# Optimization experiments

Hardware: AMD Instinct MI355X
Metric: run time of the kernel (lower is better)

Reference implementation:

```python
import jax, jax.numpy as jnp
import numpy as np

N, K, C, J = 200000, 512, 64, 32  # nodes, node feature dim, mixture components (Ccurr+1), macrostates


def setup_inputs() -> dict:
    key = jax.random.key(0)
    k0, k1, k2, k3, k4, k5 = jax.random.split(key, 6)
    x = jax.random.normal(k0, (N, K), dtype=jnp.float32)
    macrostate = jax.random.randint(k1, (N,), 0, J)  # macrostate_assignments (int, constant)
    # Gaussian emission parameters theta[k] (diagonal covariance), one per component
    mu = jax.random.normal(k2, (C, K), dtype=jnp.float32)
    log_var = 0.1 * jax.random.normal(k3, (C, K), dtype=jnp.float32)
    # stick-breaking weights beta (positive, sums to 1) and CRF counts njk (non-negative)
    b = jax.random.uniform(k4, (C,), dtype=jnp.float32) + 1e-3
    beta = b / b.sum()
    njk = 100.0 * jax.random.uniform(k5, (J, C), dtype=jnp.float32)
    alpha = jnp.float32(1.0)
    return {"x": x, "mu": mu, "log_var": log_var, "beta": beta, "njk": njk,
            "alpha": alpha, "macrostate": macrostate}


def reference(x, mu, log_var, beta, njk, alpha, macrostate):
    # f_X_theta_log[u, k] = theta[k].get_data_log_likelihood(x[u])  (diagonal Gaussian)
    # expand ||(x - mu)/sigma||^2 as a GEMM to stay compute-bound:
    inv_var = jnp.exp(-log_var)                                   # [C, K]
    quad = ((x * x) @ inv_var.T                                   # [N, C]
            - 2.0 * (x @ (mu * inv_var).T)
            + jnp.sum(mu * mu * inv_var, axis=1))
    log_norm = jnp.sum(log_var, axis=1) + x.shape[1] * jnp.log(2.0 * jnp.pi)
    f_log = -0.5 * (quad + log_norm)                              # [N, C]
    # per-node: unnorm_log_p_zu = log(alpha*beta + njk[j]) + f_X_theta_log[u]
    prior_log = jnp.log(alpha * beta[None, :] + njk)              # [J, C]
    logits = prior_log[macrostate] + f_log                        # [N, C]
    # p_zu via numerically-stable softmax; posterior_matrix[u] += p_zu
    posterior = jax.nn.softmax(logits, axis=1)
    return posterior
```

## Files before the change

kernel.cpp:

```cpp
#include <hip/hip_runtime.h>
#include <hip/hip_bf16.h>

typedef _Float16 f16;
typedef _Float16 f16x8 __attribute__((ext_vector_type(8)));
typedef float f32x4 __attribute__((ext_vector_type(4)));

#define NN 200000
#define KK 512
#define CC 64
#define JJ 32
#define WFRAG_ELEMS (48 * 4 * 64 * 8)

__global__ __launch_bounds__(256) void fill_w(const float* __restrict__ mu,
                                              const float* __restrict__ lv,
                                              f16* __restrict__ wfrag) {
  int idx = blockIdx.x * 256 + threadIdx.x;
  int i = idx & 7, l = (idx >> 3) & 63, ct = (idx >> 9) & 3, kF = idx >> 11;
  int k = (kF & 15) * 32 + (l >> 4) * 8 + i;
  int c = ct * 16 + (l & 15);
  int sec = kF >> 4;
  float lvv = lv[c * KK + k];
  float w;
  if (sec == 0) {
    w = -0.5f * expm1f(-lvv);
  } else {
    float w2 = mu[c * KK + k] * expf(-lvv);
    float wh = (float)(f16)w2;
    w = (sec == 1) ? wh : (w2 - wh);
  }
  wfrag[idx] = (f16)w;
}

__global__ __launch_bounds__(64) void fill_bias(const float* __restrict__ mu,
                                                const float* __restrict__ lv,
                                                const float* __restrict__ beta,
                                                const float* __restrict__ njk,
                                                const float* __restrict__ alphap,
                                                float* __restrict__ bias) {
  int c = blockIdx.x;
  int lane = threadIdx.x;
  float s = 0.0f;
  for (int k = lane; k < KK; k += 64) {
    float l2 = lv[c * KK + k];
    float m = mu[c * KK + k];
    s += fmaf(m * m, expf(-l2), l2);
  }
  #pragma unroll
  for (int d = 1; d < 64; d <<= 1) s += __shfl_xor(s, d, 64);
  float base = -0.5f * (s + 512.0f * 1.8378770664093453f);
  if (lane < JJ)
    bias[lane * CC + c] = logf(alphap[0] * beta[c] + njk[lane * CC + c]) + base;
}

__global__ __launch_bounds__(64, 3) void gmm_main(
    const float* __restrict__ x, const int* __restrict__ ms,
    const f16* __restrict__ wfrag, const float* __restrict__ bias,
    float* __restrict__ out) {
  const int lane = threadIdx.x;
  const int lr = lane & 15;
  const int kg = lane >> 4;
  const int row0 = blockIdx.x * 32;

  f32x4 acc[2][4];
  #pragma unroll
  for (int rt = 0; rt < 2; ++rt)
    #pragma unroll
    for (int ct = 0; ct < 4; ++ct) acc[rt][ct] = (f32x4)0.0f;

  const float* xp0 = x + (size_t)(row0 + lr) * KK + kg * 8;
  const float* xp1 = x + (size_t)(row0 + 16 + lr) * KK + kg * 8;
  const f16* wb = wfrag + lane * 8;

  #pragma unroll 2
  for (int s = 0; s < 16; ++s) {
    f16x8 fxx[2], fxh[2], fxl[2];
    #pragma unroll
    for (int rt = 0; rt < 2; ++rt) {
      const float* xp = rt ? xp1 : xp0;
      f32x4 a = *reinterpret_cast<const f32x4*>(xp + s * 32);
      f32x4 b = *reinterpret_cast<const f32x4*>(xp + s * 32 + 4);
      #pragma unroll
      for (int i = 0; i < 8; ++i) {
        float v = (i < 4) ? a[i] : b[i - 4];
        f16 h = (f16)v;
        fxh[rt][i] = h;
        fxl[rt][i] = (f16)(v - (float)h);
        fxx[rt][i] = (f16)(v * v);
      }
    }
    f16x8 bw1[4], bwh[4], bwl[4];
    #pragma unroll
    for (int ct = 0; ct < 4; ++ct) {
      bw1[ct] = *reinterpret_cast<const f16x8*>(wb + (size_t)(((0 + s) * 4 + ct) * 64) * 8);
      bwh[ct] = *reinterpret_cast<const f16x8*>(wb + (size_t)(((16 + s) * 4 + ct) * 64) * 8);
      bwl[ct] = *reinterpret_cast<const f16x8*>(wb + (size_t)(((32 + s) * 4 + ct) * 64) * 8);
    }
    #pragma unroll
    for (int ct = 0; ct < 4; ++ct)
      #pragma unroll
      for (int rt = 0; rt < 2; ++rt) {
        acc[rt][ct] = __builtin_amdgcn_mfma_f32_16x16x32_f16(fxx[rt], bw1[ct], acc[rt][ct], 0, 0, 0);
        acc[rt][ct] = __builtin_amdgcn_mfma_f32_16x16x32_f16(fxh[rt], bwh[ct], acc[rt][ct], 0, 0, 0);
        acc[rt][ct] = __builtin_amdgcn_mfma_f32_16x16x32_f16(fxh[rt], bwl[ct], acc[rt][ct], 0, 0, 0);
        acc[rt][ct] = __builtin_amdgcn_mfma_f32_16x16x32_f16(fxl[rt], bwh[ct], acc[rt][ct], 0, 0, 0);
      }
  }

  #pragma unroll
  for (int rt = 0; rt < 2; ++rt) {
    int rbase = row0 + rt * 16 + kg * 4;
    #pragma unroll
    for (int r = 0; r < 4; ++r) {
      int j = ms[rbase + r];
      const float* bj = bias + j * CC + lr;
      float v0 = acc[rt][0][r] + bj[0];
      float v1 = acc[rt][1][r] + bj[16];
      float v2 = acc[rt][2][r] + bj[32];
      float v3 = acc[rt][3][r] + bj[48];
      float m = fmaxf(fmaxf(v0, v1), fmaxf(v2, v3));
      #pragma unroll
      for (int d = 1; d < 16; d <<= 1) m = fmaxf(m, __shfl_xor(m, d, 64));
      float e0 = __expf(v0 - m), e1 = __expf(v1 - m);
      float e2 = __expf(v2 - m), e3 = __expf(v3 - m);
      float sum = (e0 + e1) + (e2 + e3);
      #pragma unroll
      for (int d = 1; d < 16; d <<= 1) sum += __shfl_xor(sum, d, 64);
      float inv = 1.0f / sum;
      float* o = out + (size_t)(rbase + r) * CC + lr;
      o[0]  = e0 * inv;
      o[16] = e1 * inv;
      o[32] = e2 * inv;
      o[48] = e3 * inv;
    }
  }
}

extern "C" void kernel_launch(void* const* d_in, const int* in_sizes, int n_in,
                              void* d_out, int out_size, void* d_ws, size_t ws_size,
                              hipStream_t stream) {
  const float* x     = (const float*)d_in[0];
  const float* mu    = (const float*)d_in[1];
  const float* lv    = (const float*)d_in[2];
  const float* beta  = (const float*)d_in[3];
  const float* njk   = (const float*)d_in[4];
  const float* alpha = (const float*)d_in[5];
  const int*   ms    = (const int*)d_in[6];
  float* out = (float*)d_out;

  f16* wfrag  = (f16*)d_ws;
  float* bias = (float*)((char*)d_ws + WFRAG_ELEMS * sizeof(f16));

  fill_w<<<WFRAG_ELEMS / 256, 256, 0, stream>>>(mu, lv, wfrag);
  fill_bias<<<CC, 64, 0, stream>>>(mu, lv, beta, njk, alpha, bias);
  gmm_main<<<NN / 32, 64, 0, stream>>>(x, ms, wfrag, bias, out);
}
```

Measured before the change: 158.7 us.

## Prefetch x one K-step ahead, pack 4 waves per block, use nontemporal I/O

```diff
diff --git a/kernel.cpp b/kernel.cpp
--- a/kernel.cpp
+++ b/kernel.cpp
@@ -52,14 +52,16 @@
     bias[lane * CC + c] = logf(alphap[0] * beta[c] + njk[lane * CC + c]) + base;
 }
 
-__global__ __launch_bounds__(64, 3) void gmm_main(
+__global__ __launch_bounds__(256, 4) void gmm_main(
     const float* __restrict__ x, const int* __restrict__ ms,
     const f16* __restrict__ wfrag, const float* __restrict__ bias,
     float* __restrict__ out) {
-  const int lane = threadIdx.x;
+  const int lane = threadIdx.x & 63;
+  const int wv = threadIdx.x >> 6;
   const int lr = lane & 15;
   const int kg = lane >> 4;
-  const int row0 = blockIdx.x * 32;
+  const int row0 = blockIdx.x * 128 + wv * 32;
+  if (row0 >= NN) return;
 
   f32x4 acc[2][4];
   #pragma unroll
@@ -68,42 +70,58 @@
     for (int ct = 0; ct < 4; ++ct) acc[rt][ct] = (f32x4)0.0f;
 
   const float* xp0 = x + (size_t)(row0 + lr) * KK + kg * 8;
-  const float* xp1 = x + (size_t)(row0 + 16 + lr) * KK + kg * 8;
+  const float* xp1 = xp0 + (size_t)16 * KK;
   const f16* wb = wfrag + lane * 8;
 
-  #pragma unroll 2
+  f32x4 cx[4];
+  cx[0] = __builtin_nontemporal_load(reinterpret_cast<const f32x4*>(xp0));
+  cx[1] = __builtin_nontemporal_load(reinterpret_cast<const f32x4*>(xp0 + 4));
+  cx[2] = __builtin_nontemporal_load(reinterpret_cast<const f32x4*>(xp1));
+  cx[3] = __builtin_nontemporal_load(reinterpret_cast<const f32x4*>(xp1 + 4));
+
+  #pragma unroll 1
   for (int s = 0; s < 16; ++s) {
+    f32x4 nx[4];
+    if (s < 15) {
+      const float* p0 = xp0 + (s + 1) * 32;
+      const float* p1 = xp1 + (s + 1) * 32;
+      nx[0] = __builtin_nontemporal_load(reinterpret_cast<const f32x4*>(p0));
+      nx[1] = __builtin_nontemporal_load(reinterpret_cast<const f32x4*>(p0 + 4));
+      nx[2] = __builtin_nontemporal_load(reinterpret_cast<const f32x4*>(p1));
+      nx[3] = __builtin_nontemporal_load(reinterpret_cast<const f32x4*>(p1 + 4));
+    }
+
     f16x8 fxx[2], fxh[2], fxl[2];
     #pragma unroll
     for (int rt = 0; rt < 2; ++rt) {
-      const float* xp = rt ? xp1 : xp0;
-      f32x4 a = *reinterpret_cast<const f32x4*>(xp + s * 32);
-      f32x4 b = *reinterpret_cast<const f32x4*>(xp + s * 32 + 4);
       #pragma unroll
       for (int i = 0; i < 8; ++i) {
-        float v = (i < 4) ? a[i] : b[i - 4];
+        float v = (i < 4) ? cx[rt * 2][i] : cx[rt * 2 + 1][i - 4];
         f16 h = (f16)v;
         fxh[rt][i] = h;
         fxl[rt][i] = (f16)(v - (float)h);
         fxx[rt][i] = (f16)(v * v);
       }
     }
-    f16x8 bw1[4], bwh[4], bwl[4];
+
+    const f16* wbs = wb + (size_t)s * 2048;
     #pragma unroll
     for (int ct = 0; ct < 4; ++ct) {
-      bw1[ct] = *reinterpret_cast<const f16x8*>(wb + (size_t)(((0 + s) * 4 + ct) * 64) * 8);
-      bwh[ct] = *reinterpret_cast<const f16x8*>(wb + (size_t)(((16 + s) * 4 + ct) * 64) * 8);
-      bwl[ct] = *reinterpret_cast<const f16x8*>(wb + (size_t)(((32 + s) * 4 + ct) * 64) * 8);
-    }
-    #pragma unroll
-    for (int ct = 0; ct < 4; ++ct)
+      f16x8 bw1 = *reinterpret_cast<const f16x8*>(wbs + ct * 512);
+      f16x8 bwh = *reinterpret_cast<const f16x8*>(wbs + 32768 + ct * 512);
+      f16x8 bwl = *reinterpret_cast<const f16x8*>(wbs + 65536 + ct * 512);
       #pragma unroll
       for (int rt = 0; rt < 2; ++rt) {
-        acc[rt][ct] = __builtin_amdgcn_mfma_f32_16x16x32_f16(fxx[rt], bw1[ct], acc[rt][ct], 0, 0, 0);
-        acc[rt][ct] = __builtin_amdgcn_mfma_f32_16x16x32_f16(fxh[rt], bwh[ct], acc[rt][ct], 0, 0, 0);
-        acc[rt][ct] = __builtin_amdgcn_mfma_f32_16x16x32_f16(fxh[rt], bwl[ct], acc[rt][ct], 0, 0, 0);
-        acc[rt][ct] = __builtin_amdgcn_mfma_f32_16x16x32_f16(fxl[rt], bwh[ct], acc[rt][ct], 0, 0, 0);
+        acc[rt][ct] = __builtin_amdgcn_mfma_f32_16x16x32_f16(fxx[rt], bw1, acc[rt][ct], 0, 0, 0);
+        acc[rt][ct] = __builtin_amdgcn_mfma_f32_16x16x32_f16(fxh[rt], bwh, acc[rt][ct], 0, 0, 0);
+        acc[rt][ct] = __builtin_amdgcn_mfma_f32_16x16x32_f16(fxh[rt], bwl, acc[rt][ct], 0, 0, 0);
+        acc[rt][ct] = __builtin_amdgcn_mfma_f32_16x16x32_f16(fxl[rt], bwh, acc[rt][ct], 0, 0, 0);
       }
+    }
+
+    if (s < 15) {
+      cx[0] = nx[0]; cx[1] = nx[1]; cx[2] = nx[2]; cx[3] = nx[3];
+    }
   }
 
   #pragma unroll
@@ -127,10 +145,10 @@
       for (int d = 1; d < 16; d <<= 1) sum += __shfl_xor(sum, d, 64);
       float inv = 1.0f / sum;
       float* o = out + (size_t)(rbase + r) * CC + lr;
-      o[0]  = e0 * inv;
-      o[16] = e1 * inv;
-      o[32] = e2 * inv;
-      o[48] = e3 * inv;
+      __builtin_nontemporal_store(e0 * inv, o);
+      __builtin_nontemporal_store(e1 * inv, o + 16);
+      __builtin_nontemporal_store(e2 * inv, o + 32);
+      __builtin_nontemporal_store(e3 * inv, o + 48);
     }
   }
 }
@@ -152,5 +170,5 @@
 
   fill_w<<<WFRAG_ELEMS / 256, 256, 0, stream>>>(mu, lv, wfrag);
   fill_bias<<<CC, 64, 0, stream>>>(mu, lv, beta, njk, alpha, bias);
-  gmm_main<<<NN / 32, 64, 0, stream>>>(x, ms, wfrag, bias, out);
+  gmm_main<<<(NN + 127) / 128, 256, 0, stream>>>(x, ms, wfrag, bias, out);
 }
```

New measurement: 158.8 us. About the same (+0.1%).
